# Performance work log

Hardware: AMD Instinct MI355X
Metric: run time of the kernel (lower is better)

Reference implementation:

```python
import jax, jax.numpy as jnp
import numpy as np

SIZE = 100
NUM_PARAMS = 5
DEPTH = 10            # complete binary tree: 2**DEPTH - 1 = 1023 nodes, 512 leaves
NUM_TREES = 1024
NUM_NODES = 2 ** DEPTH - 1


def setup_inputs() -> dict:
    key = jax.random.key(0)
    ks = jax.random.split(key, 7)
    times = jax.random.uniform(ks[0], (NUM_TREES, NUM_NODES), dtype=jnp.float32) + 0.1
    # Linear(1, size): weight column vector + bias
    Qw = jax.random.normal(ks[1], (SIZE,), dtype=jnp.float32) * 0.5
    Qb = jax.random.normal(ks[2], (SIZE,), dtype=jnp.float32) * 0.1
    # Linear(size, size): scaled so deep relu chain stays stable
    Ww = jax.random.normal(ks[3], (SIZE, SIZE), dtype=jnp.float32) * (0.5 / np.sqrt(SIZE))
    Wb = jax.random.normal(ks[4], (SIZE,), dtype=jnp.float32) * 0.1
    # Linear(size, num_params)
    Pw = jax.random.normal(ks[5], (NUM_PARAMS, SIZE), dtype=jnp.float32) * (1.0 / np.sqrt(SIZE))
    Pb = jax.random.normal(ks[6], (NUM_PARAMS,), dtype=jnp.float32) * 0.1
    return {"times": times, "Qw": Qw, "Qb": Qb, "Ww": Ww, "Wb": Wb, "Pw": Pw, "Pb": Pb}


def reference(times, Qw, Qb, Ww, Wb, Pw, Pb):
    """Batched, level-synchronous version of gRNN.traverse over complete binary trees.

    times: [B, 2**D - 1] node times in heap order (node i -> children 2i+1, 2i+2).
    Leaf:     h = relu(Q(t))
    Internal: h = relu(W(h_left + h_right) + Q(t))
    Root output projected to num_params. Same math as the recursive torch code.
    """
    B, N = times.shape
    D = int(np.log2(N + 1))
    # leaf level (deepest): Q(t) = t * Qw + Qb  (Linear(1, size))
    s = 2 ** (D - 1) - 1
    h = jax.nn.relu(times[:, s:s + 2 ** (D - 1), None] * Qw + Qb)  # [B, 2^(D-1), size]
    for d in range(D - 2, -1, -1):  # fixed small loop over tree depth
        s = 2 ** d - 1
        t = times[:, s:s + 2 ** d, None]                 # [B, 2^d, 1]
        comb = h[:, 0::2] + h[:, 1::2]                   # left + right children
        h = jax.nn.relu(jnp.einsum('bns,os->bno', comb, Ww) + Wb + t * Qw + Qb)
    root = h[:, 0]                                       # [B, size]
    return root @ Pw.T + Pb                              # [B, num_params]
```

## Files before the change

kernel.cpp:

```cpp
#include <hip/hip_runtime.h>

typedef _Float16 h8 __attribute__((ext_vector_type(8)));
typedef _Float16 h4 __attribute__((ext_vector_type(4)));
typedef _Float16 h2 __attribute__((ext_vector_type(2)));
typedef float f4 __attribute__((ext_vector_type(4)));

#define NT 7
#define KC 4
#define HSTRIDE 104

__global__ __launch_bounds__(64, 1)
void grnn_fused(const float* __restrict__ times,
                const float* __restrict__ Qw,
                const float* __restrict__ Qb,
                const float* __restrict__ Ww,
                const float* __restrict__ Wb,
                const float* __restrict__ Pw,
                const float* __restrict__ Pb,
                float* __restrict__ out)
{
  __shared__ __align__(16) _Float16 Cs[128][HSTRIDE];
  __shared__ __align__(16) _Float16 trash[512];
  __shared__ __align__(4)  _Float16 ts_fold[512];
  __shared__ __align__(4)  h2 tsp[256];

  const int lane = threadIdx.x;
  const int l15  = lane & 15;
  const int kg   = lane >> 4;
  const int tree = blockIdx.x;

  {
    const float* tg = times + tree * 1023;
    #pragma unroll
    for (int q = 0; q < 4; ++q) {
      const int pr = lane + 64 * q;
      *(h2*)&ts_fold[2 * pr] = (h2){(_Float16)tg[2 * pr], (_Float16)tg[2 * pr + 1]};
      tsp[pr] = (h2){(_Float16)tg[511 + 2 * pr], (_Float16)tg[512 + 2 * pr]};
    }
  }

  h8 wf[NT][KC];
  #pragma unroll
  for (int nt = 0; nt < NT; ++nt) {
    const int r = nt * 16 + l15;
    #pragma unroll
    for (int kc = 0; kc < KC; ++kc) {
      h8 v;
      #pragma unroll
      for (int j = 0; j < 8; ++j) v[j] = (_Float16)0.f;
      if (r < 100) {
        const int kb = kc * 32 + kg * 8;
        if (kc < 3) {
          const f4 w0 = *(const f4*)&Ww[r * 100 + kb];
          const f4 w1 = *(const f4*)&Ww[r * 100 + kb + 4];
          #pragma unroll
          for (int j = 0; j < 4; ++j) {
            v[j]     = (_Float16)w0[j];
            v[j + 4] = (_Float16)w1[j];
          }
        } else if (kg == 0) {
          const f4 w0 = *(const f4*)&Ww[r * 100 + 96];
          #pragma unroll
          for (int j = 0; j < 4; ++j) v[j] = (_Float16)w0[j];
          v[4] = (_Float16)Qw[r];
          v[5] = (_Float16)(Qb[r] + Wb[r]);
        }
      }
      wf[nt][kc] = v;
    }
  }

  h8 qwp[KC], qbp[KC];
  #pragma unroll
  for (int kc = 0; kc < KC; ++kc) {
    const int kb = kc * 32 + kg * 8;
    #pragma unroll
    for (int j = 0; j < 8; ++j) {
      const int ix = kb + j;
      qwp[kc][j] = (ix < 100) ? (_Float16)Qw[ix] : (_Float16)0.f;
      qbp[kc][j] = (ix < 100) ? (_Float16)Qb[ix] : (_Float16)0.f;
    }
  }

#define DO_MT(AFR, MT) do {                                                   \
    const int rw_ = (MT) * 8 + (l15 >> 1);                                    \
    _Float16* pv_ = (l15 & 1) ? &trash[lane * 4] : &Cs[rw_][kg * 4];          \
    _Float16* p6_ = kg ? &trash[lane * 4] : pv_;                              \
    _Pragma("unroll")                                                         \
    for (int nt_ = 0; nt_ < NT; ++nt_) {                                      \
      f4 acc_ = {0.f, 0.f, 0.f, 0.f};                                         \
      _Pragma("unroll")                                                       \
      for (int kc_ = 0; kc_ < KC; ++kc_)                                      \
        acc_ = __builtin_amdgcn_mfma_f32_16x16x32_f16(wf[nt_][kc_],           \
                                                      AFR[kc_], acc_, 0,0,0); \
      h2 c0_ = {(_Float16)acc_[0], (_Float16)acc_[1]};                        \
      h2 c1_ = {(_Float16)acc_[2], (_Float16)acc_[3]};                        \
      const h2 z2_ = {(_Float16)0.f, (_Float16)0.f};                          \
      c0_ = __builtin_elementwise_max(c0_, z2_);                              \
      c1_ = __builtin_elementwise_max(c1_, z2_);                              \
      int d0_ = __builtin_amdgcn_mov_dpp(__builtin_bit_cast(int, c0_),        \
                                         0xB1, 0xF, 0xF, true);               \
      int d1_ = __builtin_amdgcn_mov_dpp(__builtin_bit_cast(int, c1_),        \
                                         0xB1, 0xF, 0xF, true);               \
      c0_ = c0_ + __builtin_bit_cast(h2, d0_);                                \
      c1_ = c1_ + __builtin_bit_cast(h2, d1_);                                \
      h4 hv_ = {c0_[0], c0_[1], c1_[0], c1_[1]};                              \
      *(h4*)((nt_ == 6 ? p6_ : pv_) + nt_ * 16) = hv_;                        \
    }                                                                         \
  } while (0)

#define DO_MT_ROOT(AFR) do {                                                  \
    _Float16* pv_ = (l15 == 0) ? &Cs[0][kg * 4] : &trash[lane * 4];           \
    _Float16* p6_ = kg ? &trash[lane * 4] : pv_;                              \
    _Pragma("unroll")                                                         \
    for (int nt_ = 0; nt_ < NT; ++nt_) {                                      \
      f4 acc_ = {0.f, 0.f, 0.f, 0.f};                                         \
      _Pragma("unroll")                                                       \
      for (int kc_ = 0; kc_ < KC; ++kc_)                                      \
        acc_ = __builtin_amdgcn_mfma_f32_16x16x32_f16(wf[nt_][kc_],           \
                                                      AFR[kc_], acc_, 0,0,0); \
      h2 c0_ = {(_Float16)acc_[0], (_Float16)acc_[1]};                        \
      h2 c1_ = {(_Float16)acc_[2], (_Float16)acc_[3]};                        \
      const h2 z2_ = {(_Float16)0.f, (_Float16)0.f};                          \
      c0_ = __builtin_elementwise_max(c0_, z2_);                              \
      c1_ = __builtin_elementwise_max(c1_, z2_);                              \
      h4 hv_ = {c0_[0], c0_[1], c1_[0], c1_[1]};                              \
      *(h4*)((nt_ == 6 ? p6_ : pv_) + nt_ * 16) = hv_;                        \
    }                                                                         \
  } while (0)

#define LOAD_AFR(AFR, MT, S) do {                                             \
    const int row_ = (MT) * 16 + l15;                                         \
    AFR[0] = *(const h8*)&Cs[row_][kg * 8];                                   \
    AFR[1] = *(const h8*)&Cs[row_][32 + kg * 8];                              \
    AFR[2] = *(const h8*)&Cs[row_][64 + kg * 8];                              \
    h4 lo_ = *(const h4*)&Cs[row_][96];                                       \
    h4 hi_ = {ts_fold[(S) + (MT) * 16 + l15], (_Float16)1.f,                  \
              (_Float16)0.f, (_Float16)0.f};                                  \
    AFR[3] = __builtin_shufflevector(lo_, hi_, 0, 1, 2, 3, 4, 5, 6, 7);       \
  } while (0)

  const h8 z8 = {(_Float16)0.f, (_Float16)0.f, (_Float16)0.f, (_Float16)0.f,
                 (_Float16)0.f, (_Float16)0.f, (_Float16)0.f, (_Float16)0.f};
  #pragma unroll 2
  for (int i = 0; i < 16; ++i) {
    const int m = i * 16 + l15;
    const h2 tp = tsp[m];
    const _Float16 t0 = tp[0], t1 = tp[1];
    h8 afl[KC];
    #pragma unroll
    for (int kc = 0; kc < KC; ++kc) {
      h8 a = qwp[kc] * t0 + qbp[kc];
      h8 b = qwp[kc] * t1 + qbp[kc];
      a = __builtin_elementwise_max(a, z8);
      b = __builtin_elementwise_max(b, z8);
      afl[kc] = a + b;
    }
    afl[3][4] = ts_fold[255 + m];
    afl[3][5] = (_Float16)1.f;
    DO_MT(afl, i);
  }

  h8 af[KC], afn[KC];
  LOAD_AFR(af, 0, 127);
  #pragma unroll 1
  for (int j = 0; j < 14; ++j) {
    const int i = j - ((j < 8) ? 0 : (j < 12) ? 8 : 12);
    if (j < 13) {
      const int j2 = j + 1;
      const int d2 = (j2 < 8) ? 7 : (j2 < 12) ? 6 : 5;
      const int i2 = j2 - ((j2 < 8) ? 0 : (j2 < 12) ? 8 : 12);
      LOAD_AFR(afn, i2, (1 << d2) - 1);
    }
    DO_MT(af, i);
    if (j == 13) LOAD_AFR(afn, 0, 15);
    #pragma unroll
    for (int c = 0; c < KC; ++c) af[c] = afn[c];
  }

  #pragma unroll 1
  for (int d = 4; d >= 1; --d) {
    DO_MT(af, 0);
    LOAD_AFR(afn, 0, (1 << (d - 1)) - 1);
    #pragma unroll
    for (int c = 0; c < KC; ++c) af[c] = afn[c];
  }

  DO_MT_ROOT(af);

  #pragma unroll 1
  for (int p = 0; p < 5; ++p) {
    float v = (float)Cs[0][lane] * Pw[p * 100 + lane];
    if (lane < 36) v += (float)Cs[0][64 + lane] * Pw[p * 100 + 64 + lane];
    v += __shfl_xor(v, 32, 64);
    v += __shfl_xor(v, 16, 64);
    v += __shfl_xor(v, 8, 64);
    v += __shfl_xor(v, 4, 64);
    v += __shfl_xor(v, 2, 64);
    v += __shfl_xor(v, 1, 64);
    if (lane == 0) out[tree * 5 + p] = v + Pb[p];
  }
#undef DO_MT
#undef DO_MT_ROOT
#undef LOAD_AFR
}

extern "C" void kernel_launch(void* const* d_in, const int* in_sizes, int n_in,
                              void* d_out, int out_size, void* d_ws, size_t ws_size,
                              hipStream_t stream) {
  (void)n_in; (void)out_size; (void)d_ws; (void)ws_size;
  const float* times = (const float*)d_in[0];
  const float* Qw = (const float*)d_in[1];
  const float* Qb = (const float*)d_in[2];
  const float* Ww = (const float*)d_in[3];
  const float* Wb = (const float*)d_in[4];
  const float* Pw = (const float*)d_in[5];
  const float* Pb = (const float*)d_in[6];
  float* outp = (float*)d_out;
  const int B = in_sizes[0] / 1023;
  grnn_fused<<<dim3(B), dim3(64), 0, stream>>>(times, Qw, Qb, Ww, Wb, Pw, Pb, outp);
}
```

Before: 93.74 us.

## Split output column tiles across four waves per tree with ping-pong LDS buffers

Each tree's block grows from one wavefront to four. Each wave holds weight fragments for only two of the seven 16-column output tiles, cutting per-wave register use and serial MFMA work per level. Level results alternate between two LDS buffers with __syncthreads between levels, since all waves now write disjoint columns of a shared buffer. Node times are folded into spare padding columns of the A buffer. The cost is block barriers at every level and unequal work, because one wave owns only one tile.

Measured after the change: 95.11 us. About the same (+1.5%).

```diff
diff --git a/kernel.cpp b/kernel.cpp
--- a/kernel.cpp
+++ b/kernel.cpp
@@ -5,11 +5,10 @@
 typedef _Float16 h2 __attribute__((ext_vector_type(2)));
 typedef float f4 __attribute__((ext_vector_type(4)));
 
-#define NT 7
 #define KC 4
 #define HSTRIDE 104
 
-__global__ __launch_bounds__(64, 1)
+__global__ __launch_bounds__(256, 4)
 void grnn_fused(const float* __restrict__ times,
                 const float* __restrict__ Qw,
                 const float* __restrict__ Qb,
@@ -19,29 +18,35 @@
                 const float* __restrict__ Pb,
                 float* __restrict__ out)
 {
-  __shared__ __align__(16) _Float16 Cs[128][HSTRIDE];
-  __shared__ __align__(16) _Float16 trash[512];
-  __shared__ __align__(4)  _Float16 ts_fold[512];
-  __shared__ __align__(4)  h2 tsp[256];
-
-  const int lane = threadIdx.x;
+  __shared__ __align__(16) _Float16 Abuf[128 * HSTRIDE];
+  __shared__ __align__(16) _Float16 Bbuf[64 * HSTRIDE];
+  __shared__ __align__(16) _Float16 trash[256];
+
+  const int tid  = threadIdx.x;
+  const int lane = tid & 63;
+  const int w    = tid >> 6;
   const int l15  = lane & 15;
   const int kg   = lane >> 4;
   const int tree = blockIdx.x;
+  const bool two = (w < 3);
+
+  _Float16* const Af = Abuf;
+  _Float16* const Bf = Bbuf;
 
   {
     const float* tg = times + tree * 1023;
-    #pragma unroll
-    for (int q = 0; q < 4; ++q) {
-      const int pr = lane + 64 * q;
-      *(h2*)&ts_fold[2 * pr] = (h2){(_Float16)tg[2 * pr], (_Float16)tg[2 * pr + 1]};
-      tsp[pr] = (h2){(_Float16)tg[511 + 2 * pr], (_Float16)tg[512 + 2 * pr]};
-    }
-  }
-
-  h8 wf[NT][KC];
+    Af[(tid >> 2) * HSTRIDE + 100 + (tid & 3)] = (_Float16)tg[tid];
+    if (tid < 255) {
+      const int i = tid + 256;
+      Af[(i >> 2) * HSTRIDE + 100 + (i & 3)] = (_Float16)tg[i];
+    }
+    ((h2*)Bf)[tid] = (h2){(_Float16)tg[511 + 2 * tid], (_Float16)tg[512 + 2 * tid]};
+  }
+
+  h8 wf[2][KC];
   #pragma unroll
-  for (int nt = 0; nt < NT; ++nt) {
+  for (int s = 0; s < 2; ++s) {
+    const int nt = w + 4 * s;
     const int r = nt * 16 + l15;
     #pragma unroll
     for (int kc = 0; kc < KC; ++kc) {
@@ -66,7 +71,7 @@
           v[5] = (_Float16)(Qb[r] + Wb[r]);
         }
       }
-      wf[nt][kc] = v;
+      wf[s][kc] = v;
     }
   }
 
@@ -82,16 +87,18 @@
     }
   }
 
-#define DO_MT(AFR, MT) do {                                                   \
-    const int rw_ = (MT) * 8 + (l15 >> 1);                                    \
-    _Float16* pv_ = (l15 & 1) ? &trash[lane * 4] : &Cs[rw_][kg * 4];          \
-    _Float16* p6_ = kg ? &trash[lane * 4] : pv_;                              \
+  __syncthreads();
+
+#define DO_MT(AFR, DSTP, MT) do {                                             \
+    _Float16* pv_ = (DSTP) + ((MT) * 8 + (l15 >> 1)) * HSTRIDE + kg * 4;      \
     _Pragma("unroll")                                                         \
-    for (int nt_ = 0; nt_ < NT; ++nt_) {                                      \
+    for (int s_ = 0; s_ < 2; ++s_) {                                          \
+      if (s_ && !two) break;                                                  \
+      const int nt_ = w + 4 * s_;                                             \
       f4 acc_ = {0.f, 0.f, 0.f, 0.f};                                         \
       _Pragma("unroll")                                                       \
       for (int kc_ = 0; kc_ < KC; ++kc_)                                      \
-        acc_ = __builtin_amdgcn_mfma_f32_16x16x32_f16(wf[nt_][kc_],           \
+        acc_ = __builtin_amdgcn_mfma_f32_16x16x32_f16(wf[s_][kc_],            \
                                                       AFR[kc_], acc_, 0,0,0); \
       h2 c0_ = {(_Float16)acc_[0], (_Float16)acc_[1]};                        \
       h2 c1_ = {(_Float16)acc_[2], (_Float16)acc_[3]};                        \
@@ -105,19 +112,21 @@
       c0_ = c0_ + __builtin_bit_cast(h2, d0_);                                \
       c1_ = c1_ + __builtin_bit_cast(h2, d1_);                                \
       h4 hv_ = {c0_[0], c0_[1], c1_[0], c1_[1]};                              \
-      *(h4*)((nt_ == 6 ? p6_ : pv_) + nt_ * 16) = hv_;                        \
+      _Float16* p_ = ((nt_ == 6) & (kg != 0)) ? &trash[lane * 4]              \
+                                              : pv_ + nt_ * 16;               \
+      *(h4*)p_ = hv_;                                                         \
     }                                                                         \
   } while (0)
 
 #define DO_MT_ROOT(AFR) do {                                                  \
-    _Float16* pv_ = (l15 == 0) ? &Cs[0][kg * 4] : &trash[lane * 4];           \
-    _Float16* p6_ = kg ? &trash[lane * 4] : pv_;                              \
     _Pragma("unroll")                                                         \
-    for (int nt_ = 0; nt_ < NT; ++nt_) {                                      \
+    for (int s_ = 0; s_ < 2; ++s_) {                                          \
+      if (s_ && !two) break;                                                  \
+      const int nt_ = w + 4 * s_;                                             \
       f4 acc_ = {0.f, 0.f, 0.f, 0.f};                                         \
       _Pragma("unroll")                                                       \
       for (int kc_ = 0; kc_ < KC; ++kc_)                                      \
-        acc_ = __builtin_amdgcn_mfma_f32_16x16x32_f16(wf[nt_][kc_],           \
+        acc_ = __builtin_amdgcn_mfma_f32_16x16x32_f16(wf[s_][kc_],            \
                                                       AFR[kc_], acc_, 0,0,0); \
       h2 c0_ = {(_Float16)acc_[0], (_Float16)acc_[1]};                        \
       h2 c1_ = {(_Float16)acc_[2], (_Float16)acc_[3]};                        \
@@ -125,73 +134,99 @@
       c0_ = __builtin_elementwise_max(c0_, z2_);                              \
       c1_ = __builtin_elementwise_max(c1_, z2_);                              \
       h4 hv_ = {c0_[0], c0_[1], c1_[0], c1_[1]};                              \
-      *(h4*)((nt_ == 6 ? p6_ : pv_) + nt_ * 16) = hv_;                        \
+      _Float16* p_ = ((l15 == 0) & !((nt_ == 6) & (kg != 0)))                 \
+                         ? Af + nt_ * 16 + kg * 4 : &trash[lane * 4];         \
+      *(h4*)p_ = hv_;                                                         \
     }                                                                         \
   } while (0)
 
-#define LOAD_AFR(AFR, MT, S) do {                                             \
-    const int row_ = (MT) * 16 + l15;                                         \
-    AFR[0] = *(const h8*)&Cs[row_][kg * 8];                                   \
-    AFR[1] = *(const h8*)&Cs[row_][32 + kg * 8];                              \
-    AFR[2] = *(const h8*)&Cs[row_][64 + kg * 8];                              \
-    h4 lo_ = *(const h4*)&Cs[row_][96];                                       \
-    h4 hi_ = {ts_fold[(S) + (MT) * 16 + l15], (_Float16)1.f,                  \
+#define LOAD_AFR(AFR, SRCP, MT, S) do {                                       \
+    const int rb_ = ((MT) * 16 + l15) * HSTRIDE;                              \
+    AFR[0] = *(const h8*)((SRCP) + rb_ + kg * 8);                             \
+    AFR[1] = *(const h8*)((SRCP) + rb_ + 32 + kg * 8);                        \
+    AFR[2] = *(const h8*)((SRCP) + rb_ + 64 + kg * 8);                        \
+    h4 lo_ = *(const h4*)((SRCP) + rb_ + 96);                                 \
+    const int ti_ = (S) + (MT) * 16 + l15;                                    \
+    h4 hi_ = {Af[(ti_ >> 2) * HSTRIDE + 100 + (ti_ & 3)], (_Float16)1.f,      \
               (_Float16)0.f, (_Float16)0.f};                                  \
     AFR[3] = __builtin_shufflevector(lo_, hi_, 0, 1, 2, 3, 4, 5, 6, 7);       \
   } while (0)
 
-  const h8 z8 = {(_Float16)0.f, (_Float16)0.f, (_Float16)0.f, (_Float16)0.f,
-                 (_Float16)0.f, (_Float16)0.f, (_Float16)0.f, (_Float16)0.f};
-  #pragma unroll 2
-  for (int i = 0; i < 16; ++i) {
-    const int m = i * 16 + l15;
-    const h2 tp = tsp[m];
-    const _Float16 t0 = tp[0], t1 = tp[1];
-    h8 afl[KC];
-    #pragma unroll
-    for (int kc = 0; kc < KC; ++kc) {
-      h8 a = qwp[kc] * t0 + qbp[kc];
-      h8 b = qwp[kc] * t1 + qbp[kc];
-      a = __builtin_elementwise_max(a, z8);
-      b = __builtin_elementwise_max(b, z8);
-      afl[kc] = a + b;
-    }
-    afl[3][4] = ts_fold[255 + m];
-    afl[3][5] = (_Float16)1.f;
-    DO_MT(afl, i);
-  }
+  {
+    const h8 z8 = {(_Float16)0.f, (_Float16)0.f, (_Float16)0.f, (_Float16)0.f,
+                   (_Float16)0.f, (_Float16)0.f, (_Float16)0.f, (_Float16)0.f};
+    const h2* tsp = (const h2*)Bf;
+    #pragma unroll 2
+    for (int i = 0; i < 16; ++i) {
+      const int m = i * 16 + l15;
+      const h2 tp = tsp[m];
+      const _Float16 t0 = tp[0], t1 = tp[1];
+      h8 afl[KC];
+      #pragma unroll
+      for (int kc = 0; kc < KC; ++kc) {
+        h8 a = qwp[kc] * t0 + qbp[kc];
+        h8 b = qwp[kc] * t1 + qbp[kc];
+        a = __builtin_elementwise_max(a, z8);
+        b = __builtin_elementwise_max(b, z8);
+        afl[kc] = a + b;
+      }
+      const int ti = 255 + m;
+      afl[3][4] = Af[(ti >> 2) * HSTRIDE + 100 + (ti & 3)];
+      afl[3][5] = (_Float16)1.f;
+      DO_MT(afl, Af, i);
+    }
+  }
+  __syncthreads();
 
   h8 af[KC], afn[KC];
-  LOAD_AFR(af, 0, 127);
-  #pragma unroll 1
-  for (int j = 0; j < 14; ++j) {
-    const int i = j - ((j < 8) ? 0 : (j < 12) ? 8 : 12);
-    if (j < 13) {
-      const int j2 = j + 1;
-      const int d2 = (j2 < 8) ? 7 : (j2 < 12) ? 6 : 5;
-      const int i2 = j2 - ((j2 < 8) ? 0 : (j2 < 12) ? 8 : 12);
-      LOAD_AFR(afn, i2, (1 << d2) - 1);
-    }
-    DO_MT(af, i);
-    if (j == 13) LOAD_AFR(afn, 0, 15);
+
+  LOAD_AFR(af, Af, 0, 127);
+  #pragma unroll 1
+  for (int i = 0; i < 8; ++i) {
+    if (i < 7) LOAD_AFR(afn, Af, i + 1, 127);
+    DO_MT(af, Bf, i);
     #pragma unroll
     for (int c = 0; c < KC; ++c) af[c] = afn[c];
   }
+  __syncthreads();
+
+  LOAD_AFR(af, Bf, 0, 63);
+  #pragma unroll 1
+  for (int i = 0; i < 4; ++i) {
+    if (i < 3) LOAD_AFR(afn, Bf, i + 1, 63);
+    DO_MT(af, Af, i);
+    #pragma unroll
+    for (int c = 0; c < KC; ++c) af[c] = afn[c];
+  }
+  __syncthreads();
+
+  LOAD_AFR(af, Af, 0, 31);
+  #pragma unroll 1
+  for (int i = 0; i < 2; ++i) {
+    if (i < 1) LOAD_AFR(afn, Af, 1, 31);
+    DO_MT(af, Bf, i);
+    #pragma unroll
+    for (int c = 0; c < KC; ++c) af[c] = afn[c];
+  }
+  __syncthreads();
 
   #pragma unroll 1
   for (int d = 4; d >= 1; --d) {
-    DO_MT(af, 0);
-    LOAD_AFR(afn, 0, (1 << (d - 1)) - 1);
-    #pragma unroll
-    for (int c = 0; c < KC; ++c) af[c] = afn[c];
-  }
-
+    _Float16* const srcp = (d & 1) ? Af : Bf;
+    _Float16* const dstp = (d & 1) ? Bf : Af;
+    LOAD_AFR(af, srcp, 0, (1 << d) - 1);
+    DO_MT(af, dstp, 0);
+    __syncthreads();
+  }
+
+  LOAD_AFR(af, Bf, 0, 0);
   DO_MT_ROOT(af);
-
-  #pragma unroll 1
-  for (int p = 0; p < 5; ++p) {
-    float v = (float)Cs[0][lane] * Pw[p * 100 + lane];
-    if (lane < 36) v += (float)Cs[0][64 + lane] * Pw[p * 100 + 64 + lane];
+  __syncthreads();
+
+  #pragma unroll 1
+  for (int p = w; p < 5; p += 4) {
+    float v = (float)Af[lane] * Pw[p * 100 + lane];
+    if (lane < 36) v += (float)Af[64 + lane] * Pw[p * 100 + 64 + lane];
     v += __shfl_xor(v, 32, 64);
     v += __shfl_xor(v, 16, 64);
     v += __shfl_xor(v, 8, 64);
@@ -218,5 +253,5 @@
   const float* Pb = (const float*)d_in[6];
   float* outp = (float*)d_out;
   const int B = in_sizes[0] / 1023;
-  grnn_fused<<<dim3(B), dim3(64), 0, stream>>>(times, Qw, Qb, Ww, Wb, Pw, Pb, outp);
+  grnn_fused<<<dim3(B), dim3(256), 0, stream>>>(times, Qw, Qb, Ww, Wb, Pw, Pb, outp);
 }
```

## Split each tree across two wavefronts with per-subtree shared buffers

Applied to the files above, without the earlier changes.

Each block now runs two wavefronts, and each one processes half of the tree (one root subtree) in its own shared-memory slab. The two wavefronts combine their subtree roots through a small shared row after one barrier. The LDS staging of times is removed, so times are read directly from global memory inside the loops. This halves the serial level chain per wavefront and raises the number of waves in flight. The cost is a duplicate weight-fragment register load in each wave, extra global loads of times, and the final root step being computed redundantly by both waves.

Measured after the change: 92.68 us. Within noise of the previous version (-1.1%).

```diff
diff --git a/kernel.cpp b/kernel.cpp
--- a/kernel.cpp
+++ b/kernel.cpp
@@ -9,7 +9,7 @@
 #define KC 4
 #define HSTRIDE 104
 
-__global__ __launch_bounds__(64, 1)
+__global__ __launch_bounds__(128, 2)
 void grnn_fused(const float* __restrict__ times,
                 const float* __restrict__ Qw,
                 const float* __restrict__ Qb,
@@ -19,25 +19,18 @@
                 const float* __restrict__ Pb,
                 float* __restrict__ out)
 {
-  __shared__ __align__(16) _Float16 Cs[128][HSTRIDE];
-  __shared__ __align__(16) _Float16 trash[512];
-  __shared__ __align__(4)  _Float16 ts_fold[512];
-  __shared__ __align__(4)  h2 tsp[256];
-
-  const int lane = threadIdx.x;
+  __shared__ __align__(16) _Float16 Cs[2][64][HSTRIDE];
+  __shared__ __align__(16) _Float16 Hrow[2][HSTRIDE];
+  __shared__ __align__(16) _Float16 trash[256];
+
+  const int tid  = threadIdx.x;
+  const int lane = tid & 63;
+  const int w    = tid >> 6;
   const int l15  = lane & 15;
   const int kg   = lane >> 4;
   const int tree = blockIdx.x;
-
-  {
-    const float* tg = times + tree * 1023;
-    #pragma unroll
-    for (int q = 0; q < 4; ++q) {
-      const int pr = lane + 64 * q;
-      *(h2*)&ts_fold[2 * pr] = (h2){(_Float16)tg[2 * pr], (_Float16)tg[2 * pr + 1]};
-      tsp[pr] = (h2){(_Float16)tg[511 + 2 * pr], (_Float16)tg[512 + 2 * pr]};
-    }
-  }
+  const float* tg = times + tree * 1023;
+  _Float16 (* const C)[HSTRIDE] = Cs[w];
 
   h8 wf[NT][KC];
   #pragma unroll
@@ -82,10 +75,15 @@
     }
   }
 
+  const _Float16 t_l5 = (_Float16)tg[31 + 16 * w + l15];
+  const _Float16 t_l4 = (_Float16)tg[15 + 8 * w + l15];
+  const _Float16 t_l3 = (_Float16)tg[7 + 4 * w + l15];
+  const _Float16 t_l2 = (_Float16)tg[3 + 2 * w + l15];
+  const _Float16 t_l1 = (_Float16)tg[1 + w + l15];
+  const _Float16 t_rt = (_Float16)tg[l15];
+
 #define DO_MT(AFR, MT) do {                                                   \
-    const int rw_ = (MT) * 8 + (l15 >> 1);                                    \
-    _Float16* pv_ = (l15 & 1) ? &trash[lane * 4] : &Cs[rw_][kg * 4];          \
-    _Float16* p6_ = kg ? &trash[lane * 4] : pv_;                              \
+    _Float16* pv_ = &C[(MT) * 8 + (l15 >> 1)][kg * 4];                        \
     _Pragma("unroll")                                                         \
     for (int nt_ = 0; nt_ < NT; ++nt_) {                                      \
       f4 acc_ = {0.f, 0.f, 0.f, 0.f};                                         \
@@ -105,13 +103,13 @@
       c0_ = c0_ + __builtin_bit_cast(h2, d0_);                                \
       c1_ = c1_ + __builtin_bit_cast(h2, d1_);                                \
       h4 hv_ = {c0_[0], c0_[1], c1_[0], c1_[1]};                              \
-      *(h4*)((nt_ == 6 ? p6_ : pv_) + nt_ * 16) = hv_;                        \
+      _Float16* p_ = ((nt_ == 6) & (kg != 0)) ? &trash[lane * 4]              \
+                                              : pv_ + nt_ * 16;               \
+      *(h4*)p_ = hv_;                                                         \
     }                                                                         \
   } while (0)
 
-#define DO_MT_ROOT(AFR) do {                                                  \
-    _Float16* pv_ = (l15 == 0) ? &Cs[0][kg * 4] : &trash[lane * 4];           \
-    _Float16* p6_ = kg ? &trash[lane * 4] : pv_;                              \
+#define DO_RAW(AFR, DST) do {                                                 \
     _Pragma("unroll")                                                         \
     for (int nt_ = 0; nt_ < NT; ++nt_) {                                      \
       f4 acc_ = {0.f, 0.f, 0.f, 0.f};                                         \
@@ -125,73 +123,101 @@
       c0_ = __builtin_elementwise_max(c0_, z2_);                              \
       c1_ = __builtin_elementwise_max(c1_, z2_);                              \
       h4 hv_ = {c0_[0], c0_[1], c1_[0], c1_[1]};                              \
-      *(h4*)((nt_ == 6 ? p6_ : pv_) + nt_ * 16) = hv_;                        \
+      _Float16* p_ = ((l15 == 0) & !((nt_ == 6) & (kg != 0)))                 \
+                         ? (DST) + nt_ * 16 + kg * 4 : &trash[lane * 4];      \
+      *(h4*)p_ = hv_;                                                         \
     }                                                                         \
   } while (0)
 
-#define LOAD_AFR(AFR, MT, S) do {                                             \
-    const int row_ = (MT) * 16 + l15;                                         \
-    AFR[0] = *(const h8*)&Cs[row_][kg * 8];                                   \
-    AFR[1] = *(const h8*)&Cs[row_][32 + kg * 8];                              \
-    AFR[2] = *(const h8*)&Cs[row_][64 + kg * 8];                              \
-    h4 lo_ = *(const h4*)&Cs[row_][96];                                       \
-    h4 hi_ = {ts_fold[(S) + (MT) * 16 + l15], (_Float16)1.f,                  \
+#define LOAD_AFR(AFR, MT, TBASE) do {                                         \
+    const int rr_ = (MT) * 16 + l15;                                          \
+    AFR[0] = *(const h8*)&C[rr_][kg * 8];                                     \
+    AFR[1] = *(const h8*)&C[rr_][32 + kg * 8];                                \
+    AFR[2] = *(const h8*)&C[rr_][64 + kg * 8];                                \
+    h4 lo_ = *(const h4*)&C[rr_][96];                                         \
+    h4 hi_ = {(_Float16)tg[(TBASE) + (MT) * 16 + l15], (_Float16)1.f,         \
               (_Float16)0.f, (_Float16)0.f};                                  \
     AFR[3] = __builtin_shufflevector(lo_, hi_, 0, 1, 2, 3, 4, 5, 6, 7);       \
   } while (0)
 
-  const h8 z8 = {(_Float16)0.f, (_Float16)0.f, (_Float16)0.f, (_Float16)0.f,
-                 (_Float16)0.f, (_Float16)0.f, (_Float16)0.f, (_Float16)0.f};
-  #pragma unroll 2
-  for (int i = 0; i < 16; ++i) {
-    const int m = i * 16 + l15;
-    const h2 tp = tsp[m];
-    const _Float16 t0 = tp[0], t1 = tp[1];
-    h8 afl[KC];
-    #pragma unroll
-    for (int kc = 0; kc < KC; ++kc) {
-      h8 a = qwp[kc] * t0 + qbp[kc];
-      h8 b = qwp[kc] * t1 + qbp[kc];
-      a = __builtin_elementwise_max(a, z8);
-      b = __builtin_elementwise_max(b, z8);
-      afl[kc] = a + b;
-    }
-    afl[3][4] = ts_fold[255 + m];
-    afl[3][5] = (_Float16)1.f;
-    DO_MT(afl, i);
+#define LOAD_AFR_R(AFR, MT, TREG) do {                                        \
+    const int rr_ = (MT) * 16 + l15;                                          \
+    AFR[0] = *(const h8*)&C[rr_][kg * 8];                                     \
+    AFR[1] = *(const h8*)&C[rr_][32 + kg * 8];                                \
+    AFR[2] = *(const h8*)&C[rr_][64 + kg * 8];                                \
+    h4 lo_ = *(const h4*)&C[rr_][96];                                         \
+    h4 hi_ = {(TREG), (_Float16)1.f, (_Float16)0.f, (_Float16)0.f};           \
+    AFR[3] = __builtin_shufflevector(lo_, hi_, 0, 1, 2, 3, 4, 5, 6, 7);       \
+  } while (0)
+
+  {
+    const h8 z8 = {(_Float16)0.f, (_Float16)0.f, (_Float16)0.f, (_Float16)0.f,
+                   (_Float16)0.f, (_Float16)0.f, (_Float16)0.f, (_Float16)0.f};
+    const int lb = 511 + 256 * w;
+    const int nb = 255 + 128 * w;
+    #pragma unroll 2
+    for (int i = 0; i < 8; ++i) {
+      const int m = i * 16 + l15;
+      const _Float16 t0 = (_Float16)tg[lb + 2 * m];
+      const _Float16 t1 = (_Float16)tg[lb + 2 * m + 1];
+      h8 afl[KC];
+      #pragma unroll
+      for (int kc = 0; kc < KC; ++kc) {
+        h8 a = qwp[kc] * t0 + qbp[kc];
+        h8 b = qwp[kc] * t1 + qbp[kc];
+        a = __builtin_elementwise_max(a, z8);
+        b = __builtin_elementwise_max(b, z8);
+        afl[kc] = a + b;
+      }
+      afl[3][4] = (_Float16)tg[nb + m];
+      afl[3][5] = (_Float16)1.f;
+      DO_MT(afl, i);
+    }
   }
 
   h8 af[KC], afn[KC];
-  LOAD_AFR(af, 0, 127);
+  const int b7 = 127 + 64 * w;
+  const int b6 = 63 + 32 * w;
+  LOAD_AFR(af, 0, b7);
   #pragma unroll 1
-  for (int j = 0; j < 14; ++j) {
-    const int i = j - ((j < 8) ? 0 : (j < 12) ? 8 : 12);
-    if (j < 13) {
+  for (int j = 0; j < 6; ++j) {
+    const int i = (j < 4) ? j : j - 4;
+    if (j < 5) {
       const int j2 = j + 1;
-      const int d2 = (j2 < 8) ? 7 : (j2 < 12) ? 6 : 5;
-      const int i2 = j2 - ((j2 < 8) ? 0 : (j2 < 12) ? 8 : 12);
-      LOAD_AFR(afn, i2, (1 << d2) - 1);
+      const int i2 = (j2 < 4) ? j2 : j2 - 4;
+      LOAD_AFR(afn, i2, (j2 < 4) ? b7 : b6);
     }
     DO_MT(af, i);
-    if (j == 13) LOAD_AFR(afn, 0, 15);
     #pragma unroll
     for (int c = 0; c < KC; ++c) af[c] = afn[c];
   }
 
+  LOAD_AFR_R(af, 0, t_l5); DO_MT(af, 0);
+  LOAD_AFR_R(af, 0, t_l4); DO_MT(af, 0);
+  LOAD_AFR_R(af, 0, t_l3); DO_MT(af, 0);
+  LOAD_AFR_R(af, 0, t_l2); DO_MT(af, 0);
+
+  LOAD_AFR_R(af, 0, t_l1);
+  DO_RAW(af, &Hrow[w][0]);
+
+  __syncthreads();
+
+  {
+    af[0] = *(const h8*)&Hrow[0][kg * 8]  + *(const h8*)&Hrow[1][kg * 8];
+    af[1] = *(const h8*)&Hrow[0][32 + kg * 8] + *(const h8*)&Hrow[1][32 + kg * 8];
+    af[2] = *(const h8*)&Hrow[0][64 + kg * 8] + *(const h8*)&Hrow[1][64 + kg * 8];
+    h4 lo0 = *(const h4*)&Hrow[0][96];
+    h4 lo1 = *(const h4*)&Hrow[1][96];
+    h4 lo = lo0 + lo1;
+    h4 hi = {t_rt, (_Float16)1.f, (_Float16)0.f, (_Float16)0.f};
+    af[3] = __builtin_shufflevector(lo, hi, 0, 1, 2, 3, 4, 5, 6, 7);
+  }
+  DO_RAW(af, &C[0][0]);
+
   #pragma unroll 1
-  for (int d = 4; d >= 1; --d) {
-    DO_MT(af, 0);
-    LOAD_AFR(afn, 0, (1 << (d - 1)) - 1);
-    #pragma unroll
-    for (int c = 0; c < KC; ++c) af[c] = afn[c];
-  }
-
-  DO_MT_ROOT(af);
-
-  #pragma unroll 1
-  for (int p = 0; p < 5; ++p) {
-    float v = (float)Cs[0][lane] * Pw[p * 100 + lane];
-    if (lane < 36) v += (float)Cs[0][64 + lane] * Pw[p * 100 + 64 + lane];
+  for (int p = w; p < 5; p += 2) {
+    float v = (float)C[0][lane] * Pw[p * 100 + lane];
+    if (lane < 36) v += (float)C[0][64 + lane] * Pw[p * 100 + 64 + lane];
     v += __shfl_xor(v, 32, 64);
     v += __shfl_xor(v, 16, 64);
     v += __shfl_xor(v, 8, 64);
@@ -201,8 +227,9 @@
     if (lane == 0) out[tree * 5 + p] = v + Pb[p];
   }
 #undef DO_MT
-#undef DO_MT_ROOT
+#undef DO_RAW
 #undef LOAD_AFR
+#undef LOAD_AFR_R
 }
 
 extern "C" void kernel_launch(void* const* d_in, const int* in_sizes, int n_in,
@@ -218,5 +245,5 @@
   const float* Pb = (const float*)d_in[6];
   float* outp = (float*)d_out;
   const int B = in_sizes[0] / 1023;
-  grnn_fused<<<dim3(B), dim3(64), 0, stream>>>(times, Qw, Qb, Ww, Wb, Pw, Pb, outp);
+  grnn_fused<<<dim3(B), dim3(128), 0, stream>>>(times, Qw, Qb, Ww, Wb, Pw, Pb, outp);
 }
```
